# Optimization experiments

Hardware: AMD Instinct MI355X
Metric: run time of the kernel (lower is better)

Reference implementation:

```python
import jax, jax.numpy as jnp
import numpy as np

EPS = 1e-8

def rms_norm(x, scale):
    # full RMSNorm over last dim (p < 0 branch): norm/sqrt(d)
    d = x.shape[-1]
    norm = jnp.linalg.norm(x, ord=2, axis=-1, keepdims=True)
    rms = norm * (d ** -0.5)
    return scale * (x / (rms + EPS))

def setup_inputs() -> dict:
    key = jax.random.key(0)
    ks = jax.random.split(key, 4)
    B, N, C, H = 2, 2048, 1024, 16
    hd = C // H
    x = jax.random.normal(ks[0], (B, N, C), dtype=jnp.float32)
    Wqkv = jax.random.normal(ks[1], (C, 3 * C), dtype=jnp.float32) * (C ** -0.5)
    Wproj = jax.random.normal(ks[2], (C, C), dtype=jnp.float32) * (C ** -0.5)
    bproj = jnp.zeros((C,), dtype=jnp.float32)
    q_scale = jnp.ones((hd,), dtype=jnp.float32)
    k_scale = jnp.ones((hd,), dtype=jnp.float32)
    return {"x": x, "Wqkv": Wqkv, "Wproj": Wproj, "bproj": bproj,
            "q_scale": q_scale, "k_scale": k_scale}

def reference(x, Wqkv, Wproj, bproj, q_scale, k_scale):
    B, N, C = x.shape
    H = 16
    hd = C // H
    scale = hd ** -0.5
    qkv = (x @ Wqkv).reshape(B, N, 3, H, hd)
    qkv = jnp.transpose(qkv, (2, 0, 3, 1, 4))  # t b h n c
    q, k, v = qkv[0], qkv[1], qkv[2]
    q = rms_norm(q, q_scale)
    k = rms_norm(k, k_scale)
    attn = jnp.einsum('bhnc,bhmc->bhnm', q, k) * scale
    attn = jax.nn.softmax(attn, axis=-1)
    out = jnp.einsum('bhnm,bhmc->bhnc', attn, v)
    out = jnp.transpose(out, (0, 2, 1, 3)).reshape(B, N, C)
    return out @ Wproj + bproj
```

## Files before the change

### kernel.cpp

```cpp
#include <hip/hip_runtime.h>


typedef _Float16 half_t;
typedef __attribute__((ext_vector_type(2))) __fp16 fp16x2;
typedef __attribute__((ext_vector_type(4))) _Float16 half4v;
typedef __attribute__((ext_vector_type(8))) _Float16 half8;
typedef __attribute__((ext_vector_type(4))) float f32x4;
typedef __attribute__((ext_vector_type(4))) unsigned uint4v;

#define DI __device__ __forceinline__

DI void gl_lds16(const void* g, void* l) {
    __builtin_amdgcn_global_load_lds((const __attribute__((address_space(1))) void*)g,
                                     (__attribute__((address_space(3))) void*)l, 16, 0, 0);
}

DI float exp2_fast(float x) {
    float r;
    asm("v_exp_f32 %0, %1" : "=v"(r) : "v"(x));
    return r;
}

DI void pl32_swap(unsigned& a, unsigned& b) {
    asm("v_permlane32_swap_b32 %0, %1" : "+v"(a), "+v"(b));
}
DI void pl16_swap(unsigned& a, unsigned& b) {
    asm("v_permlane16_swap_b32 %0, %1" : "+v"(a), "+v"(b));
}

DI unsigned pk_u32(float lo, float hi) {
    fp16x2 t = __builtin_amdgcn_cvt_pkrtz(lo, hi);
    return *(unsigned*)&t;
}

__global__ void prep_all(const float* __restrict__ x, const float* __restrict__ Wqkv,
                         const float* __restrict__ Wproj, half_t* __restrict__ xh,
                         half_t* __restrict__ wqt, half_t* __restrict__ wpt) {
    __shared__ float t[32][33];
    int bid = blockIdx.x;
    if (bid < 4096) {
        int i = (bid * 256 + threadIdx.x) * 4;
        float4 v = *(const float4*)(x + i);
        half4v o;
        o[0] = (half_t)v.x; o[1] = (half_t)v.y; o[2] = (half_t)v.z; o[3] = (half_t)v.w;
        *(half4v*)(xh + i) = o;
    } else if (bid < 4096 + 3072) {
        int i = bid - 4096;
        int c0 = (i % 96) * 32, r0 = (i / 96) * 32;
        int tx = threadIdx.x & 31, ty = threadIdx.x >> 5;
#pragma unroll
        for (int k = 0; k < 4; k++)
            t[ty + 8 * k][tx] = Wqkv[(size_t)(r0 + ty + 8 * k) * 3072 + c0 + tx];
        __syncthreads();
#pragma unroll
        for (int k = 0; k < 4; k++)
            wqt[(size_t)(c0 + ty + 8 * k) * 1024 + r0 + tx] = (half_t)t[tx][ty + 8 * k];
    } else {
        int i = bid - 4096 - 3072;
        int c0 = (i % 32) * 32, r0 = (i / 32) * 32;
        int tx = threadIdx.x & 31, ty = threadIdx.x >> 5;
#pragma unroll
        for (int k = 0; k < 4; k++)
            t[ty + 8 * k][tx] = Wproj[(size_t)(r0 + ty + 8 * k) * 1024 + c0 + tx];
        __syncthreads();
#pragma unroll
        for (int k = 0; k < 4; k++)
            wpt[(size_t)(c0 + ty + 8 * k) * 1024 + r0 + tx] = (half_t)t[tx][ty + 8 * k];
    }
}

__global__ __launch_bounds__(256, 4) void gemm_qkv(
    const half_t* __restrict__ A, const half_t* __restrict__ Bt,
    const float* __restrict__ qs, const float* __restrict__ ks,
    half_t* __restrict__ qh, half_t* __restrict__ kh, half_t* __restrict__ vth) {
    const int K = 1024;
    __shared__ __align__(16) half_t Al[2][128 * 32];
    __shared__ __align__(16) half_t Bl[2][128 * 32];
    int tid = threadIdx.x;
    int w = tid >> 6, l = tid & 63;
    int wr = w >> 1, wc = w & 1;
    int g = l >> 4, r = l & 15;
    int m0 = blockIdx.x * 128, n0 = blockIdx.y * 128;
    f32x4 acc[4][4] = {};

#define STAGE_QKV(kt, buf)                                                        \
    {                                                                             \
        _Pragma("unroll")                                                         \
        for (int p = 0; p < 2; p++) {                                             \
            int ci = p * 256 + tid;                                               \
            int row = ci >> 2, c = ci & 3, lc = c ^ ((row >> 1) & 3);             \
            gl_lds16(A + (size_t)(m0 + row) * K + (kt) * 32 + lc * 8,             \
                     &Al[buf][0] + ci * 8);                                       \
            gl_lds16(Bt + (size_t)(n0 + row) * K + (kt) * 32 + lc * 8,            \
                     &Bl[buf][0] + ci * 8);                                       \
        }                                                                         \
    }

    STAGE_QKV(0, 0);
    __syncthreads();
    int cur = 0;
    for (int kt = 0; kt < 32; kt++) {
        if (kt < 31) STAGE_QKV(kt + 1, cur ^ 1);
        half8 af[4], bf[4];
#pragma unroll
        for (int i = 0; i < 4; i++) {
            int row = wr * 64 + i * 16 + r;
            af[i] = *(const half8*)(&Al[cur][0] + row * 32 + ((g ^ ((row >> 1) & 3)) << 3));
            int rowb = wc * 64 + i * 16 + r;
            bf[i] = *(const half8*)(&Bl[cur][0] + rowb * 32 + ((g ^ ((rowb >> 1) & 3)) << 3));
        }
#pragma unroll
        for (int i = 0; i < 4; i++)
#pragma unroll
            for (int j = 0; j < 4; j++)
                acc[i][j] = __builtin_amdgcn_mfma_f32_16x16x32_f16(af[i], bf[j], acc[i][j], 0, 0, 0);
        __syncthreads();
        cur ^= 1;
    }

    int tsec = n0 >> 10;
    if (tsec == 2) {
#pragma unroll
        for (int i = 0; i < 4; i++)
#pragma unroll
            for (int j = 0; j < 4; j++) {
                int gcol = n0 + wc * 64 + j * 16 + r;
                int h = (gcol >> 6) & 15;
                int f = gcol & 63;
                int growb = m0 + wr * 64 + i * 16 + g * 4;
                int b = growb >> 11;
                int n = growb & 2047;
                half4v pv;
#pragma unroll
                for (int rr = 0; rr < 4; rr++) pv[rr] = (half_t)acc[i][j][rr];
                *(half4v*)(vth + ((size_t)(b * 16 + h) * 64 + f) * 2048 + n) = pv;
            }
    } else {
        const float* sc = (tsec == 0) ? qs : ks;
        half_t* dst = (tsec == 0) ? qh : kh;
        float extra = (tsec == 0) ? (0.125f * 1.44269504f) : 1.0f;
        float scv[4];
#pragma unroll
        for (int j = 0; j < 4; j++) scv[j] = sc[j * 16 + r];
#pragma unroll
        for (int i = 0; i < 4; i++)
#pragma unroll
            for (int rr = 0; rr < 4; rr++) {
                float ss = 0.f;
#pragma unroll
                for (int j = 0; j < 4; j++) ss += acc[i][j][rr] * acc[i][j][rr];
#pragma unroll
                for (int d = 1; d < 16; d <<= 1) ss += __shfl_xor(ss, d, 64);
                float inv = extra / (sqrtf(ss) * 0.125f + 1e-8f);
                int grow = m0 + wr * 64 + i * 16 + g * 4 + rr;
                int b = grow >> 11;
                int n = grow & 2047;
#pragma unroll
                for (int j = 0; j < 4; j++) {
                    int gcol = n0 + wc * 64 + j * 16 + r;
                    int h = (gcol >> 6) & 15;
                    int f = gcol & 63;
                    dst[((size_t)(b * 16 + h) * 2048 + n) * 64 + f] =
                        (half_t)(acc[i][j][rr] * inv * scv[j]);
                }
            }
    }
}

__global__ __launch_bounds__(512, 8) void attn(
    const half_t* __restrict__ qh, const half_t* __restrict__ kh,
    const half_t* __restrict__ vth, half_t* __restrict__ aoh) {
    int bh = blockIdx.y;
    int q0 = blockIdx.x * 64;
    int tid = threadIdx.x, w = tid >> 6, l = tid & 63, g = l >> 4, r = l & 15;
    int hf = w >> 2, qs = w & 3, lt = tid & 255;

    const half_t* Qp = qh + (size_t)bh * 2048 * 64;
    const half_t* Kp = kh + (size_t)bh * 2048 * 64 + (size_t)hf * 1024 * 64;
    const half_t* Vp = vth + (size_t)bh * 64 * 2048 + hf * 1024;

    __shared__ __align__(16) char smem[32768];
    half_t* Kb[2] = {(half_t*)(smem + hf * 8192), (half_t*)(smem + hf * 8192 + 4096)};
    half_t* Vb[2] = {(half_t*)(smem + 16384 + hf * 8192), (half_t*)(smem + 16384 + hf * 8192 + 4096)};

    int krow = lt >> 3, kc = lt & 7, klc = kc ^ (krow & 7);
    const half_t* kst = Kp + (size_t)krow * 64 + klc * 8;
    int vrow = lt >> 2, vc = lt & 3, vlc = vc ^ ((vrow >> 1) & 3);
    const half_t* vst = Vp + (size_t)vrow * 2048 + vlc * 8;

    int koff[4], voff[4];
#pragma unroll
    for (int ks = 0; ks < 2; ks++)
#pragma unroll
        for (int tt = 0; tt < 2; tt++) {
            int row = tt * 16 + r;
            koff[ks * 2 + tt] = row * 64 + (((ks * 4 + g) ^ (row & 7)) << 3);
        }
#pragma unroll
    for (int cf = 0; cf < 4; cf++) {
        int row = cf * 16 + r;
        voff[cf] = row * 32 + ((g ^ ((row >> 1) & 3)) << 3);
    }

    half8 qf[2];
#pragma unroll
    for (int ks = 0; ks < 2; ks++)
        qf[ks] = *(const half8*)(Qp + (size_t)(q0 + qs * 16 + r) * 64 + ks * 32 + g * 8);

    f32x4 o[4] = {};
    float m = -1e30f, lsum = 0.f;

    gl_lds16(kst, Kb[0] + lt * 8);
    gl_lds16(vst, Vb[0] + lt * 8);
    __syncthreads();

#define ATTN_TILE(BUF, T)                                                          \
    {                                                                              \
        if ((T) < 31) {                                                            \
            gl_lds16(kst + ((T) + 1) * 2048, Kb[(BUF) ^ 1] + lt * 8);              \
            gl_lds16(vst + ((T) + 1) * 32, Vb[(BUF) ^ 1] + lt * 8);                \
        }                                                                          \
        const half_t* Kc = Kb[BUF];                                                \
        const half_t* Vc = Vb[BUF];                                                \
        f32x4 s[2] = {};                                                           \
        _Pragma("unroll")                                                          \
        for (int ks = 0; ks < 2; ks++)                                             \
            _Pragma("unroll")                                                      \
            for (int tt = 0; tt < 2; tt++) {                                       \
                half8 kf = *(const half8*)(Kc + koff[ks * 2 + tt]);                \
                s[tt] = __builtin_amdgcn_mfma_f32_16x16x32_f16(kf, qf[ks], s[tt], 0, 0, 0); \
            }                                                                      \
        float thr = m + 11.0f;                                                     \
        bool ok = true;                                                            \
        _Pragma("unroll")                                                          \
        for (int tt = 0; tt < 2; tt++)                                             \
            _Pragma("unroll")                                                      \
            for (int e = 0; e < 4; e++) ok = ok && (s[tt][e] <= thr);              \
        if (!__all(ok)) {                                                          \
            float mx = fmaxf(fmaxf(s[0][0], s[0][1]), fmaxf(s[0][2], s[0][3]));    \
            mx = fmaxf(mx, fmaxf(fmaxf(s[1][0], s[1][1]), fmaxf(s[1][2], s[1][3]))); \
            mx = fmaxf(mx, __shfl_xor(mx, 16, 64));                                \
            mx = fmaxf(mx, __shfl_xor(mx, 32, 64));                                \
            float mn = fmaxf(m, mx);                                               \
            float fac = exp2_fast(m - mn);                                         \
            lsum *= fac;                                                           \
            _Pragma("unroll")                                                      \
            for (int cf = 0; cf < 4; cf++) {                                       \
                o[cf][0] *= fac; o[cf][1] *= fac; o[cf][2] *= fac; o[cf][3] *= fac; \
            }                                                                      \
            m = mn;                                                                \
        }                                                                          \
        _Pragma("unroll")                                                          \
        for (int tt = 0; tt < 2; tt++)                                             \
            _Pragma("unroll")                                                      \
            for (int e = 0; e < 4; e++) {                                          \
                float p = exp2_fast(s[tt][e] - m);                                 \
                s[tt][e] = p;                                                      \
                lsum += p;                                                         \
            }                                                                      \
        unsigned b0 = pk_u32(s[0][0], s[0][1]);                                    \
        unsigned b1 = pk_u32(s[0][2], s[0][3]);                                    \
        unsigned b2 = pk_u32(s[1][0], s[1][1]);                                    \
        unsigned b3 = pk_u32(s[1][2], s[1][3]);                                    \
        pl32_swap(b0, b2); pl16_swap(b0, b2);                                      \
        pl32_swap(b1, b3); pl16_swap(b1, b3);                                      \
        uint4v pw; pw[0] = b0; pw[1] = b1; pw[2] = b2; pw[3] = b3;                 \
        half8 pf = *(half8*)&pw;                                                   \
        _Pragma("unroll")                                                          \
        for (int cf = 0; cf < 4; cf++) {                                           \
            half8 vf = *(const half8*)(Vc + voff[cf]);                             \
            o[cf] = __builtin_amdgcn_mfma_f32_16x16x32_f16(vf, pf, o[cf], 0, 0, 0); \
        }                                                                          \
        __syncthreads();                                                           \
    }

    for (int t = 0; t < 32; t += 2) {
        ATTN_TILE(0, t);
        ATTN_TILE(1, t + 1);
    }

    lsum += __shfl_xor(lsum, 16, 64);
    lsum += __shfl_xor(lsum, 32, 64);

    float* mo = (float*)smem;
    float* mml = (float*)(smem + 17408);
    int q2 = qs * 16 + r;
    if (hf) {
#pragma unroll
        for (int cf = 0; cf < 4; cf++)
            *(f32x4*)(mo + q2 * 68 + cf * 16 + g * 4) = o[cf];
        if (l < 16) {
            mml[q2 * 2] = m;
            mml[q2 * 2 + 1] = lsum;
        }
    }
    __syncthreads();
    if (!hf) {
        float m1 = mml[q2 * 2], ls1 = mml[q2 * 2 + 1];
        float M = fmaxf(m, m1);
        float w0 = exp2_fast(m - M), w1 = exp2_fast(m1 - M);
        float inv = 1.0f / (w0 * lsum + w1 * ls1);
        w0 *= inv; w1 *= inv;
        int n = q0 + q2;
        int b = bh >> 4, h = bh & 15;
#pragma unroll
        for (int cf = 0; cf < 4; cf++) {
            f32x4 o1 = *(const f32x4*)(mo + q2 * 68 + cf * 16 + g * 4);
            half4v ov;
#pragma unroll
            for (int e = 0; e < 4; e++) ov[e] = (half_t)(o[cf][e] * w0 + o1[e] * w1);
            *(half4v*)(aoh + ((size_t)b * 2048 + n) * 1024 + h * 64 + cf * 16 + g * 4) = ov;
        }
    }
}

__global__ __launch_bounds__(256, 4) void gemm_proj(
    const half_t* __restrict__ A, const half_t* __restrict__ Bt,
    const float* __restrict__ bias, float* __restrict__ out) {
    const int K = 1024;
    __shared__ __align__(16) half_t Al[2][64 * 32];
    __shared__ __align__(16) half_t Bl[2][128 * 32];
    int tid = threadIdx.x, w = tid >> 6, l = tid & 63;
    int wr = w >> 1, wc = w & 1, g = l >> 4, r = l & 15;
    int m0 = blockIdx.x * 64, n0 = blockIdx.y * 128;
    f32x4 acc[2][4] = {};

#define STAGE_PROJ(kt, buf)                                                       \
    {                                                                             \
        {                                                                         \
            int ci = tid;                                                         \
            int row = ci >> 2, c = ci & 3, lc = c ^ ((row >> 1) & 3);             \
            gl_lds16(A + (size_t)(m0 + row) * K + (kt) * 32 + lc * 8,             \
                     &Al[buf][0] + ci * 8);                                       \
        }                                                                         \
        _Pragma("unroll")                                                         \
        for (int p = 0; p < 2; p++) {                                             \
            int ci = p * 256 + tid;                                               \
            int row = ci >> 2, c = ci & 3, lc = c ^ ((row >> 1) & 3);             \
            gl_lds16(Bt + (size_t)(n0 + row) * K + (kt) * 32 + lc * 8,            \
                     &Bl[buf][0] + ci * 8);                                       \
        }                                                                         \
    }

    STAGE_PROJ(0, 0);
    __syncthreads();
    int cur = 0;
    for (int kt = 0; kt < 32; kt++) {
        if (kt < 31) STAGE_PROJ(kt + 1, cur ^ 1);
        half8 af[2], bf[4];
#pragma unroll
        for (int i = 0; i < 2; i++) {
            int row = wr * 32 + i * 16 + r;
            af[i] = *(const half8*)(&Al[cur][0] + row * 32 + ((g ^ ((row >> 1) & 3)) << 3));
        }
#pragma unroll
        for (int j = 0; j < 4; j++) {
            int rowb = wc * 64 + j * 16 + r;
            bf[j] = *(const half8*)(&Bl[cur][0] + rowb * 32 + ((g ^ ((rowb >> 1) & 3)) << 3));
        }
#pragma unroll
        for (int i = 0; i < 2; i++)
#pragma unroll
            for (int j = 0; j < 4; j++)
                acc[i][j] = __builtin_amdgcn_mfma_f32_16x16x32_f16(af[i], bf[j], acc[i][j], 0, 0, 0);
        __syncthreads();
        cur ^= 1;
    }

#pragma unroll
    for (int i = 0; i < 2; i++)
#pragma unroll
        for (int j = 0; j < 4; j++) {
            int gcol = n0 + wc * 64 + j * 16 + r;
            float bv = bias[gcol];
#pragma unroll
            for (int rr = 0; rr < 4; rr++) {
                int grow = m0 + wr * 32 + i * 16 + g * 4 + rr;
                out[(size_t)grow * 1024 + gcol] = acc[i][j][rr] + bv;
            }
        }
}

extern "C" void kernel_launch(void* const* d_in, const int* in_sizes, int n_in,
                              void* d_out, int out_size, void* d_ws, size_t ws_size,
                              hipStream_t stream) {
    const float* x = (const float*)d_in[0];
    const float* Wqkv = (const float*)d_in[1];
    const float* Wproj = (const float*)d_in[2];
    const float* bproj = (const float*)d_in[3];
    const float* qscale = (const float*)d_in[4];
    const float* kscale = (const float*)d_in[5];
    float* out = (float*)d_out;

    char* ws = (char*)d_ws;
    half_t* xh  = (half_t*)(ws + 0);
    half_t* wqt = (half_t*)(ws + 8388608);
    half_t* wpt = (half_t*)(ws + 14680064);
    half_t* qh  = (half_t*)(ws + 16777216);
    half_t* kh  = (half_t*)(ws + 25165824);
    half_t* vth = (half_t*)(ws + 33554432);
    half_t* aoh = (half_t*)(ws + 41943040);

    prep_all<<<8192, 256, 0, stream>>>(x, Wqkv, Wproj, xh, wqt, wpt);
    gemm_qkv<<<dim3(32, 24), 256, 0, stream>>>(xh, wqt, qscale, kscale, qh, kh, vth);
    attn<<<dim3(32, 32), 512, 0, stream>>>(qh, kh, vth, aoh);
    gemm_proj<<<dim3(64, 8), 256, 0, stream>>>(aoh, wpt, bproj, out);
}
```

Baseline: 123.6 us.

## Fuse x fp32-to-fp16 conversion into QKV GEMM A-tile loading

Removes the elementwise conversion of x from the prep kernel and has the QKV GEMM load fp32 x directly into registers, pack to fp16, and write the swizzled LDS tile after the MFMA block. This removes the intermediate half-precision x buffer write and read. In exchange, each column-block re-reads fp32 A, doubling A bytes per tile. It also adds register pressure and a register-staged path instead of direct global-to-LDS loads for A.

```diff
diff --git a/kernel.cpp b/kernel.cpp
--- a/kernel.cpp
+++ b/kernel.cpp
@@ -33,19 +33,12 @@
     return *(unsigned*)&t;
 }
 
-__global__ void prep_all(const float* __restrict__ x, const float* __restrict__ Wqkv,
-                         const float* __restrict__ Wproj, half_t* __restrict__ xh,
+__global__ void prep_all(const float* __restrict__ Wqkv, const float* __restrict__ Wproj,
                          half_t* __restrict__ wqt, half_t* __restrict__ wpt) {
     __shared__ float t[32][33];
     int bid = blockIdx.x;
-    if (bid < 4096) {
-        int i = (bid * 256 + threadIdx.x) * 4;
-        float4 v = *(const float4*)(x + i);
-        half4v o;
-        o[0] = (half_t)v.x; o[1] = (half_t)v.y; o[2] = (half_t)v.z; o[3] = (half_t)v.w;
-        *(half4v*)(xh + i) = o;
-    } else if (bid < 4096 + 3072) {
-        int i = bid - 4096;
+    if (bid < 3072) {
+        int i = bid;
         int c0 = (i % 96) * 32, r0 = (i / 96) * 32;
         int tx = threadIdx.x & 31, ty = threadIdx.x >> 5;
 #pragma unroll
@@ -56,7 +49,7 @@
         for (int k = 0; k < 4; k++)
             wqt[(size_t)(c0 + ty + 8 * k) * 1024 + r0 + tx] = (half_t)t[tx][ty + 8 * k];
     } else {
-        int i = bid - 4096 - 3072;
+        int i = bid - 3072;
         int c0 = (i % 32) * 32, r0 = (i / 32) * 32;
         int tx = threadIdx.x & 31, ty = threadIdx.x >> 5;
 #pragma unroll
@@ -70,7 +63,7 @@
 }
 
 __global__ __launch_bounds__(256, 4) void gemm_qkv(
-    const half_t* __restrict__ A, const half_t* __restrict__ Bt,
+    const float* __restrict__ X, const half_t* __restrict__ Bt,
     const float* __restrict__ qs, const float* __restrict__ ks,
     half_t* __restrict__ qh, half_t* __restrict__ kh, half_t* __restrict__ vth) {
     const int K = 1024;
@@ -83,24 +76,65 @@
     int m0 = blockIdx.x * 128, n0 = blockIdx.y * 128;
     f32x4 acc[4][4] = {};
 
-#define STAGE_QKV(kt, buf)                                                        \
+    int arow[2], alc[2];
+    const float* asrc[2];
+#pragma unroll
+    for (int p = 0; p < 2; p++) {
+        int ci = p * 256 + tid;
+        arow[p] = ci >> 2;
+        int seg = ci & 3;
+        alc[p] = seg ^ ((arow[p] >> 1) & 3);
+        asrc[p] = X + (size_t)(m0 + arow[p]) * K + seg * 8;
+    }
+
+#define STAGE_B(kt, buf)                                                          \
     {                                                                             \
         _Pragma("unroll")                                                         \
         for (int p = 0; p < 2; p++) {                                             \
             int ci = p * 256 + tid;                                               \
             int row = ci >> 2, c = ci & 3, lc = c ^ ((row >> 1) & 3);             \
-            gl_lds16(A + (size_t)(m0 + row) * K + (kt) * 32 + lc * 8,             \
-                     &Al[buf][0] + ci * 8);                                       \
             gl_lds16(Bt + (size_t)(n0 + row) * K + (kt) * 32 + lc * 8,            \
                      &Bl[buf][0] + ci * 8);                                       \
         }                                                                         \
     }
 
-    STAGE_QKV(0, 0);
+#define LOAD_A(a0, a1)                                                            \
+    {                                                                             \
+        _Pragma("unroll")                                                         \
+        for (int p = 0; p < 2; p++) {                                             \
+            a0[p] = *(const f32x4*)(asrc[p]);                                     \
+            a1[p] = *(const f32x4*)(asrc[p] + 4);                                 \
+            asrc[p] += 32;                                                        \
+        }                                                                         \
+    }
+
+#define WRITE_A(a0, a1, buf)                                                      \
+    {                                                                             \
+        _Pragma("unroll")                                                         \
+        for (int p = 0; p < 2; p++) {                                             \
+            uint4v hv;                                                            \
+            hv[0] = pk_u32(a0[p][0], a0[p][1]);                                   \
+            hv[1] = pk_u32(a0[p][2], a0[p][3]);                                   \
+            hv[2] = pk_u32(a1[p][0], a1[p][1]);                                   \
+            hv[3] = pk_u32(a1[p][2], a1[p][3]);                                   \
+            *(uint4v*)(&Al[buf][0] + arow[p] * 32 + alc[p] * 8) = hv;             \
+        }                                                                         \
+    }
+
+    {
+        f32x4 a0[2], a1[2];
+        LOAD_A(a0, a1);
+        STAGE_B(0, 0);
+        WRITE_A(a0, a1, 0);
+    }
     __syncthreads();
     int cur = 0;
     for (int kt = 0; kt < 32; kt++) {
-        if (kt < 31) STAGE_QKV(kt + 1, cur ^ 1);
+        f32x4 a0[2], a1[2];
+        if (kt < 31) {
+            LOAD_A(a0, a1);
+            STAGE_B(kt + 1, cur ^ 1);
+        }
         half8 af[4], bf[4];
 #pragma unroll
         for (int i = 0; i < 4; i++) {
@@ -114,6 +148,7 @@
 #pragma unroll
             for (int j = 0; j < 4; j++)
                 acc[i][j] = __builtin_amdgcn_mfma_f32_16x16x32_f16(af[i], bf[j], acc[i][j], 0, 0, 0);
+        if (kt < 31) WRITE_A(a0, a1, cur ^ 1);
         __syncthreads();
         cur ^= 1;
     }
@@ -393,7 +428,6 @@
     float* out = (float*)d_out;
 
     char* ws = (char*)d_ws;
-    half_t* xh  = (half_t*)(ws + 0);
     half_t* wqt = (half_t*)(ws + 8388608);
     half_t* wpt = (half_t*)(ws + 14680064);
     half_t* qh  = (half_t*)(ws + 16777216);
@@ -401,8 +435,8 @@
     half_t* vth = (half_t*)(ws + 33554432);
     half_t* aoh = (half_t*)(ws + 41943040);
 
-    prep_all<<<8192, 256, 0, stream>>>(x, Wqkv, Wproj, xh, wqt, wpt);
-    gemm_qkv<<<dim3(32, 24), 256, 0, stream>>>(xh, wqt, qscale, kscale, qh, kh, vth);
+    prep_all<<<4096, 256, 0, stream>>>(Wqkv, Wproj, wqt, wpt);
+    gemm_qkv<<<dim3(32, 24), 256, 0, stream>>>(x, wqt, qscale, kscale, qh, kh, vth);
     attn<<<dim3(32, 32), 512, 0, stream>>>(qh, kh, vth, aoh);
     gemm_proj<<<dim3(64, 8), 256, 0, stream>>>(aoh, wpt, bproj, out);
 }
```

Measured after the change: 127.2 us. 1.03x slower.
